# Optimization experiments

Hardware: AMD Instinct MI355X
Metric: run time of the kernel (lower is better)

Reference implementation:

```python
import jax, jax.numpy as jnp
import numpy as np

BITS = 8
CLIP_BOUND = 2.0 ** (BITS - 1) - 1.0  # 127 for int8
EPS = 1e-12


def _per_tensor_scale(x):
    # Dynamic per-tensor abs-max calibration (TensorQuantizer.update with
    # calibration over the whole tensor): scale maps abs-max to the clip bound.
    amax = jnp.max(jnp.abs(x))
    return CLIP_BOUND / jnp.maximum(amax, EPS)


def setup_inputs() -> dict:
    key = jax.random.key(0)
    k1, k2 = jax.random.split(key)
    lhs = jax.random.normal(k1, (4096, 4096), dtype=jnp.float32)
    rhs = jax.random.normal(k2, (4096, 4096), dtype=jnp.float32)
    return {"lhs": lhs, "rhs": rhs}


def reference(lhs, rhs):
    # --- calibration (scales are statistics, no gradient flows through them) ---
    ls = _per_tensor_scale(lhs)
    rs = _per_tensor_scale(rhs)

    # --- quantize to int8 grid ---
    ql = jnp.clip(jnp.round(lhs * ls), -CLIP_BOUND, CLIP_BOUND).astype(jnp.int8)
    qr = jnp.clip(jnp.round(rhs * rs), -CLIP_BOUND, CLIP_BOUND).astype(jnp.int8)

    # --- integer dot_general with int32 accumulation (aqt_dot_general core) ---
    dimension_numbers = (((1,), (0,)), ((), ()))
    acc = jax.lax.dot_general(
        ql, qr, dimension_numbers, preferred_element_type=jnp.int32
    )

    # --- dequantize by product of scales ---
    out = acc.astype(jnp.float32) / (ls * rs)
    return out
```

## Files before the change

kernel.cpp:

```cpp
#include <hip/hip_runtime.h>
#include <stdint.h>


#define NROW 4096
#define NELEM (4096 * 4096)

typedef __attribute__((ext_vector_type(4))) int int32x4;
typedef __attribute__((ext_vector_type(16))) int int32x16;
typedef const __attribute__((address_space(1))) int8_t* gptr1_t;
typedef __attribute__((address_space(3))) int8_t* lptr3_t;

__global__ void absmax_both_kernel(const float* __restrict__ lhs,
                                   const float* __restrict__ rhs,
                                   unsigned* __restrict__ amax) {
    __shared__ float red[4];
    const int t = blockIdx.x & 1;
    const float4* x4 = (const float4*)(t ? rhs : lhs);
    const int bid = blockIdx.x >> 1;
    const int stride = (gridDim.x >> 1) * blockDim.x;
    int i = bid * blockDim.x + threadIdx.x;
    float m0 = 0.0f, m1 = 0.0f, m2 = 0.0f, m3 = 0.0f;
    for (; i + 3 * stride < NELEM / 4; i += 4 * stride) {
        float4 a = x4[i];
        float4 b = x4[i + stride];
        float4 c = x4[i + 2 * stride];
        float4 d = x4[i + 3 * stride];
        m0 = fmaxf(m0, fmaxf(fmaxf(fabsf(a.x), fabsf(a.y)),
                             fmaxf(fabsf(a.z), fabsf(a.w))));
        m1 = fmaxf(m1, fmaxf(fmaxf(fabsf(b.x), fabsf(b.y)),
                             fmaxf(fabsf(b.z), fabsf(b.w))));
        m2 = fmaxf(m2, fmaxf(fmaxf(fabsf(c.x), fabsf(c.y)),
                             fmaxf(fabsf(c.z), fabsf(c.w))));
        m3 = fmaxf(m3, fmaxf(fmaxf(fabsf(d.x), fabsf(d.y)),
                             fmaxf(fabsf(d.z), fabsf(d.w))));
    }
    for (; i < NELEM / 4; i += stride) {
        float4 a = x4[i];
        m0 = fmaxf(m0, fmaxf(fmaxf(fabsf(a.x), fabsf(a.y)),
                             fmaxf(fabsf(a.z), fabsf(a.w))));
    }
    float m = fmaxf(fmaxf(m0, m1), fmaxf(m2, m3));
    for (int off = 32; off > 0; off >>= 1)
        m = fmaxf(m, __shfl_down(m, off, 64));
    const int lane = threadIdx.x & 63, wave = threadIdx.x >> 6;
    if (lane == 0) red[wave] = m;
    __syncthreads();
    if (threadIdx.x == 0) {
        float b = fmaxf(fmaxf(red[0], red[1]), fmaxf(red[2], red[3]));
        atomicMax(amax + t, __float_as_uint(b));
    }
}

__device__ __forceinline__ int q8(float v, float s) {
    int r = __float2int_rn(v * s);
    r = r < -127 ? -127 : r;
    r = r > 127 ? 127 : r;
    return r;
}

__device__ __forceinline__ int pack4(float a, float b, float c, float d,
                                     float s) {
    return (q8(a, s) & 0xff) | ((q8(b, s) & 0xff) << 8) |
           ((q8(c, s) & 0xff) << 16) | ((q8(d, s) & 0xff) << 24);
}

__global__ void quant_kernel(const float* __restrict__ lhs,
                             const float* __restrict__ rhs,
                             int8_t* __restrict__ qA, int8_t* __restrict__ qT,
                             const unsigned* __restrict__ amax) {
    __shared__ int8_t sm[64][68];
    if (blockIdx.x < 4096) {
        const float s = 127.0f / fmaxf(__uint_as_float(amax[0]), 1e-12f);
        const int c = blockIdx.x * 256 + threadIdx.x;
        const int l = c & 63;
        const int ks_g = (c >> 6) & 127;
        const int mt_g = c >> 13;
        const int row = mt_g * 32 + (l & 31);
        const int kb = ks_g * 32 + (l >> 5) * 16;
        const float4* src = (const float4*)(lhs + (size_t)row * NROW + kb);
        float4 v0 = src[0], v1 = src[1], v2 = src[2], v3 = src[3];
        int4 w;
        w.x = pack4(v0.x, v0.y, v0.z, v0.w, s);
        w.y = pack4(v1.x, v1.y, v1.z, v1.w, s);
        w.z = pack4(v2.x, v2.y, v2.z, v2.w, s);
        w.w = pack4(v3.x, v3.y, v3.z, v3.w, s);
        *(int4*)(qA + (size_t)c * 16) = w;
    } else {
        const float s = 127.0f / fmaxf(__uint_as_float(amax[1]), 1e-12f);
        const int b = blockIdx.x - 4096;
        const int n0 = (b & 63) * 64, k0 = (b >> 6) * 64;
        const int rl = threadIdx.x >> 4;
        const int nq = threadIdx.x & 15;
        for (int r = 0; r < 4; ++r) {
            const int kl = r * 16 + rl;
            float4 v = *(const float4*)(rhs + (size_t)(k0 + kl) * NROW + n0 + nq * 4);
            sm[nq * 4 + 0][kl] = (int8_t)q8(v.x, s);
            sm[nq * 4 + 1][kl] = (int8_t)q8(v.y, s);
            sm[nq * 4 + 2][kl] = (int8_t)q8(v.z, s);
            sm[nq * 4 + 3][kl] = (int8_t)q8(v.w, s);
        }
        __syncthreads();
        const int nt_l = threadIdx.x >> 7;
        const int ks_l = (threadIdx.x >> 6) & 1;
        const int l = threadIdx.x & 63;
        const int n_loc = nt_l * 32 + (l & 31);
        const int k_loc = ks_l * 32 + (l >> 5) * 16;
        int4 w;
        w.x = *(const int*)&sm[n_loc][k_loc + 0];
        w.y = *(const int*)&sm[n_loc][k_loc + 4];
        w.z = *(const int*)&sm[n_loc][k_loc + 8];
        w.w = *(const int*)&sm[n_loc][k_loc + 12];
        const int nt_g = (b & 63) * 2 + nt_l;
        const int ks_g = (b >> 6) * 2 + ks_l;
        *(int4*)(qT + (((size_t)nt_g * 128 + ks_g) * 64 + l) * 16) = w;
    }
}

__global__ __launch_bounds__(256, 2) void gemm_i8_kernel(
    const int8_t* __restrict__ qA, const int8_t* __restrict__ qBT,
    float* __restrict__ out, const unsigned* __restrict__ amax) {
    __shared__ __align__(16) int8_t sA[2][32768];

    const int tid = threadIdx.x;
    const int lane = tid & 63;
    const int wn = tid >> 6;

    const int bid = blockIdx.y * 16 + blockIdx.x;
    const int swz = (bid & 7) * 64 + (bid >> 3);
    const int m0 = (swz >> 4) * 128, n0 = (swz & 15) * 256;

    const int rl = lane & 31;
    const int hi = lane >> 5;

    const gptr1_t pA0 = (gptr1_t)(qA + (size_t)(m0 / 32) * 131072 + tid * 16);
    int8_t* sAf = &sA[0][0];
    const int dst0 = tid * 16;

    auto stage = [&](int slot, int w1) {
#pragma unroll
        for (int h = 0; h < 2; ++h) {
            const int kb = (2 * w1 + h) * 4096;
#pragma unroll
            for (int j = 0; j < 4; ++j) {
                __builtin_amdgcn_global_load_lds(
                    pA0 + (size_t)j * 131072 + kb,
                    (lptr3_t)(sAf + slot * 32768 + h * 16384 + dst0 + j * 4096),
                    16, 0, 0);
            }
        }
    };

    const int8_t* pbW = qBT + (size_t)(n0 / 32 + wn * 2) * 131072 + lane * 16;

    int32x16 acc[4][2];
#pragma unroll
    for (int mt = 0; mt < 4; ++mt)
#pragma unroll
        for (int nt = 0; nt < 2; ++nt) acc[mt][nt] = (int32x16)(0);

    const int aBase = lane * 16;

    int32x4 B0[4], B1[4];

#define LOADB(B, KT, KS0)                                                     \
    {                                                                         \
        const int8_t* bp = pbW + (size_t)(KT)*4096 + (KS0)*1024;              \
        B[0] = *(const int32x4*)(bp);                                         \
        B[1] = *(const int32x4*)(bp + 1024);                                  \
        B[2] = *(const int32x4*)(bp + 131072);                                \
        B[3] = *(const int32x4*)(bp + 131072 + 1024);                         \
    }

#define HALF(APTR, B, KS0)                                                    \
    {                                                                         \
        _Pragma("unroll") for (int k = 0; k < 2; ++k) {                       \
            int32x4 af[4];                                                    \
            _Pragma("unroll") for (int mt = 0; mt < 4; ++mt) af[mt] =         \
                *(const int32x4*)((APTR) + aBase + mt * 4096 +                \
                                  ((KS0) + k) * 1024);                        \
            __builtin_amdgcn_s_setprio(1);                                    \
            _Pragma("unroll") for (int mt = 0; mt < 4; ++mt)                  \
                _Pragma("unroll") for (int nt = 0; nt < 2; ++nt)              \
                    acc[mt][nt] = __builtin_amdgcn_mfma_i32_32x32x32_i8(      \
                        af[mt], B[nt * 2 + k], acc[mt][nt], 0, 0, 0);         \
            __builtin_amdgcn_s_setprio(0);                                    \
        }                                                                     \
    }

    stage(0, 0);
    __builtin_amdgcn_sched_barrier(0);
    LOADB(B0, 0, 0)
    asm volatile("s_waitcnt vmcnt(0)" ::: "memory");
    __builtin_amdgcn_sched_barrier(0);
    __builtin_amdgcn_s_barrier();
    __builtin_amdgcn_sched_barrier(0);

#pragma unroll 1
    for (int w = 0; w < 15; ++w) {
        const int8_t* a0 = sAf + (w & 1) * 32768;
        const int8_t* a1 = a0 + 16384;
        stage((w + 1) & 1, w + 1);
        __builtin_amdgcn_sched_barrier(0);
        LOADB(B1, 2 * w, 2)
        HALF(a0, B0, 0)
        LOADB(B0, 2 * w + 1, 0)
        HALF(a0, B1, 2)
        LOADB(B1, 2 * w + 1, 2)
        HALF(a1, B0, 0)
        LOADB(B0, 2 * w + 2, 0)
        HALF(a1, B1, 2)
        asm volatile("s_waitcnt vmcnt(4)" ::: "memory");
        __builtin_amdgcn_sched_barrier(0);
        __builtin_amdgcn_s_barrier();
        __builtin_amdgcn_sched_barrier(0);
    }
    {
        const int8_t* a0 = sAf + 32768;
        const int8_t* a1 = a0 + 16384;
        LOADB(B1, 30, 2)
        HALF(a0, B0, 0)
        LOADB(B0, 31, 0)
        HALF(a0, B1, 2)
        LOADB(B1, 31, 2)
        HALF(a1, B0, 0)
        HALF(a1, B1, 2)
    }

    const float ls = 127.0f / fmaxf(__uint_as_float(amax[0]), 1e-12f);
    const float rs = 127.0f / fmaxf(__uint_as_float(amax[1]), 1e-12f);
    const float inv = 1.0f / (ls * rs);
#pragma unroll
    for (int mt = 0; mt < 4; ++mt)
#pragma unroll
        for (int nt = 0; nt < 2; ++nt)
#pragma unroll
            for (int reg = 0; reg < 16; ++reg) {
                const int row = m0 + mt * 32 + (reg & 3) + 8 * (reg >> 2) +
                                4 * hi;
                const int col = n0 + wn * 64 + nt * 32 + rl;
                out[(size_t)row * NROW + col] = (float)acc[mt][nt][reg] * inv;
            }
#undef LOADB
#undef HALF
}

extern "C" void kernel_launch(void* const* d_in, const int* in_sizes, int n_in,
                              void* d_out, int out_size, void* d_ws,
                              size_t ws_size, hipStream_t stream) {
    const float* lhs = (const float*)d_in[0];
    const float* rhs = (const float*)d_in[1];
    float* out = (float*)d_out;

    int8_t* qA = (int8_t*)d_ws;
    int8_t* qBT = qA + (size_t)16 * 1024 * 1024;
    unsigned* amax = (unsigned*)(qBT + (size_t)16 * 1024 * 1024);

    hipMemsetAsync(amax, 0, 8, stream);
    absmax_both_kernel<<<2048, 256, 0, stream>>>(lhs, rhs, amax);
    quant_kernel<<<4096 + 4096, 256, 0, stream>>>(lhs, rhs, qA, qBT, amax);
    gemm_i8_kernel<<<dim3(16, 32), 256, 0, stream>>>(qA, qBT, out, amax);
}
```

Baseline: 137.7 us.

## Fuse absmax and quantize kernels into one cooperative kernel with grid sync

```diff
diff --git a/kernel.cpp b/kernel.cpp
--- a/kernel.cpp
+++ b/kernel.cpp
@@ -1,5 +1,8 @@
 #include <hip/hip_runtime.h>
+#include <hip/hip_cooperative_groups.h>
 #include <stdint.h>
+
+namespace cg = cooperative_groups;
 
 
 #define NROW 4096
@@ -9,47 +12,6 @@
 typedef __attribute__((ext_vector_type(16))) int int32x16;
 typedef const __attribute__((address_space(1))) int8_t* gptr1_t;
 typedef __attribute__((address_space(3))) int8_t* lptr3_t;
-
-__global__ void absmax_both_kernel(const float* __restrict__ lhs,
-                                   const float* __restrict__ rhs,
-                                   unsigned* __restrict__ amax) {
-    __shared__ float red[4];
-    const int t = blockIdx.x & 1;
-    const float4* x4 = (const float4*)(t ? rhs : lhs);
-    const int bid = blockIdx.x >> 1;
-    const int stride = (gridDim.x >> 1) * blockDim.x;
-    int i = bid * blockDim.x + threadIdx.x;
-    float m0 = 0.0f, m1 = 0.0f, m2 = 0.0f, m3 = 0.0f;
-    for (; i + 3 * stride < NELEM / 4; i += 4 * stride) {
-        float4 a = x4[i];
-        float4 b = x4[i + stride];
-        float4 c = x4[i + 2 * stride];
-        float4 d = x4[i + 3 * stride];
-        m0 = fmaxf(m0, fmaxf(fmaxf(fabsf(a.x), fabsf(a.y)),
-                             fmaxf(fabsf(a.z), fabsf(a.w))));
-        m1 = fmaxf(m1, fmaxf(fmaxf(fabsf(b.x), fabsf(b.y)),
-                             fmaxf(fabsf(b.z), fabsf(b.w))));
-        m2 = fmaxf(m2, fmaxf(fmaxf(fabsf(c.x), fabsf(c.y)),
-                             fmaxf(fabsf(c.z), fabsf(c.w))));
-        m3 = fmaxf(m3, fmaxf(fmaxf(fabsf(d.x), fabsf(d.y)),
-                             fmaxf(fabsf(d.z), fabsf(d.w))));
-    }
-    for (; i < NELEM / 4; i += stride) {
-        float4 a = x4[i];
-        m0 = fmaxf(m0, fmaxf(fmaxf(fabsf(a.x), fabsf(a.y)),
-                             fmaxf(fabsf(a.z), fabsf(a.w))));
-    }
-    float m = fmaxf(fmaxf(m0, m1), fmaxf(m2, m3));
-    for (int off = 32; off > 0; off >>= 1)
-        m = fmaxf(m, __shfl_down(m, off, 64));
-    const int lane = threadIdx.x & 63, wave = threadIdx.x >> 6;
-    if (lane == 0) red[wave] = m;
-    __syncthreads();
-    if (threadIdx.x == 0) {
-        float b = fmaxf(fmaxf(red[0], red[1]), fmaxf(red[2], red[3]));
-        atomicMax(amax + t, __float_as_uint(b));
-    }
-}
 
 __device__ __forceinline__ int q8(float v, float s) {
     int r = __float2int_rn(v * s);
@@ -64,55 +26,106 @@
            ((q8(c, s) & 0xff) << 16) | ((q8(d, s) & 0xff) << 24);
 }
 
-__global__ void quant_kernel(const float* __restrict__ lhs,
-                             const float* __restrict__ rhs,
-                             int8_t* __restrict__ qA, int8_t* __restrict__ qT,
-                             const unsigned* __restrict__ amax) {
+__global__ void fused_pre_kernel(const float* __restrict__ lhs,
+                                 const float* __restrict__ rhs,
+                                 int8_t* __restrict__ qA,
+                                 int8_t* __restrict__ qT,
+                                 unsigned* __restrict__ amax) {
     __shared__ int8_t sm[64][68];
-    if (blockIdx.x < 4096) {
+    __shared__ float red[4];
+
+    {
+        const int t = blockIdx.x & 1;
+        const float4* x4 = (const float4*)(t ? rhs : lhs);
+        const int bid = blockIdx.x >> 1;
+        const int stride = (gridDim.x >> 1) * blockDim.x;
+        int i = bid * blockDim.x + threadIdx.x;
+        float m0 = 0.0f, m1 = 0.0f, m2 = 0.0f, m3 = 0.0f;
+        for (; i + 3 * stride < NELEM / 4; i += 4 * stride) {
+            float4 a = x4[i];
+            float4 b = x4[i + stride];
+            float4 c = x4[i + 2 * stride];
+            float4 d = x4[i + 3 * stride];
+            m0 = fmaxf(m0, fmaxf(fmaxf(fabsf(a.x), fabsf(a.y)),
+                                 fmaxf(fabsf(a.z), fabsf(a.w))));
+            m1 = fmaxf(m1, fmaxf(fmaxf(fabsf(b.x), fabsf(b.y)),
+                                 fmaxf(fabsf(b.z), fabsf(b.w))));
+            m2 = fmaxf(m2, fmaxf(fmaxf(fabsf(c.x), fabsf(c.y)),
+                                 fmaxf(fabsf(c.z), fabsf(c.w))));
+            m3 = fmaxf(m3, fmaxf(fmaxf(fabsf(d.x), fabsf(d.y)),
+                                 fmaxf(fabsf(d.z), fabsf(d.w))));
+        }
+        for (; i < NELEM / 4; i += stride) {
+            float4 a = x4[i];
+            m0 = fmaxf(m0, fmaxf(fmaxf(fabsf(a.x), fabsf(a.y)),
+                                 fmaxf(fabsf(a.z), fabsf(a.w))));
+        }
+        float m = fmaxf(fmaxf(m0, m1), fmaxf(m2, m3));
+        for (int off = 32; off > 0; off >>= 1)
+            m = fmaxf(m, __shfl_down(m, off, 64));
+        const int lane = threadIdx.x & 63, wave = threadIdx.x >> 6;
+        if (lane == 0) red[wave] = m;
+        __syncthreads();
+        if (threadIdx.x == 0) {
+            float b = fmaxf(fmaxf(red[0], red[1]), fmaxf(red[2], red[3]));
+            atomicMax(amax + t, __float_as_uint(b));
+        }
+    }
+
+    cg::this_grid().sync();
+
+    if (blockIdx.x < 512) {
         const float s = 127.0f / fmaxf(__uint_as_float(amax[0]), 1e-12f);
-        const int c = blockIdx.x * 256 + threadIdx.x;
-        const int l = c & 63;
-        const int ks_g = (c >> 6) & 127;
-        const int mt_g = c >> 13;
-        const int row = mt_g * 32 + (l & 31);
-        const int kb = ks_g * 32 + (l >> 5) * 16;
-        const float4* src = (const float4*)(lhs + (size_t)row * NROW + kb);
-        float4 v0 = src[0], v1 = src[1], v2 = src[2], v3 = src[3];
-        int4 w;
-        w.x = pack4(v0.x, v0.y, v0.z, v0.w, s);
-        w.y = pack4(v1.x, v1.y, v1.z, v1.w, s);
-        w.z = pack4(v2.x, v2.y, v2.z, v2.w, s);
-        w.w = pack4(v3.x, v3.y, v3.z, v3.w, s);
-        *(int4*)(qA + (size_t)c * 16) = w;
+#pragma unroll 1
+        for (int it = 0; it < 8; ++it) {
+            const int c = (blockIdx.x * 8 + it) * 256 + threadIdx.x;
+            const int l = c & 63;
+            const int ks_g = (c >> 6) & 127;
+            const int mt_g = c >> 13;
+            const int row = mt_g * 32 + (l & 31);
+            const int kb = ks_g * 32 + (l >> 5) * 16;
+            const float4* src = (const float4*)(lhs + (size_t)row * NROW + kb);
+            float4 v0 = src[0], v1 = src[1], v2 = src[2], v3 = src[3];
+            int4 w;
+            w.x = pack4(v0.x, v0.y, v0.z, v0.w, s);
+            w.y = pack4(v1.x, v1.y, v1.z, v1.w, s);
+            w.z = pack4(v2.x, v2.y, v2.z, v2.w, s);
+            w.w = pack4(v3.x, v3.y, v3.z, v3.w, s);
+            *(int4*)(qA + (size_t)c * 16) = w;
+        }
     } else {
         const float s = 127.0f / fmaxf(__uint_as_float(amax[1]), 1e-12f);
-        const int b = blockIdx.x - 4096;
-        const int n0 = (b & 63) * 64, k0 = (b >> 6) * 64;
-        const int rl = threadIdx.x >> 4;
-        const int nq = threadIdx.x & 15;
-        for (int r = 0; r < 4; ++r) {
-            const int kl = r * 16 + rl;
-            float4 v = *(const float4*)(rhs + (size_t)(k0 + kl) * NROW + n0 + nq * 4);
-            sm[nq * 4 + 0][kl] = (int8_t)q8(v.x, s);
-            sm[nq * 4 + 1][kl] = (int8_t)q8(v.y, s);
-            sm[nq * 4 + 2][kl] = (int8_t)q8(v.z, s);
-            sm[nq * 4 + 3][kl] = (int8_t)q8(v.w, s);
-        }
-        __syncthreads();
-        const int nt_l = threadIdx.x >> 7;
-        const int ks_l = (threadIdx.x >> 6) & 1;
-        const int l = threadIdx.x & 63;
-        const int n_loc = nt_l * 32 + (l & 31);
-        const int k_loc = ks_l * 32 + (l >> 5) * 16;
-        int4 w;
-        w.x = *(const int*)&sm[n_loc][k_loc + 0];
-        w.y = *(const int*)&sm[n_loc][k_loc + 4];
-        w.z = *(const int*)&sm[n_loc][k_loc + 8];
-        w.w = *(const int*)&sm[n_loc][k_loc + 12];
-        const int nt_g = (b & 63) * 2 + nt_l;
-        const int ks_g = (b >> 6) * 2 + ks_l;
-        *(int4*)(qT + (((size_t)nt_g * 128 + ks_g) * 64 + l) * 16) = w;
+#pragma unroll 1
+        for (int it = 0; it < 8; ++it) {
+            const int b = (blockIdx.x - 512) * 8 + it;
+            const int n0 = (b & 63) * 64, k0 = (b >> 6) * 64;
+            const int rl = threadIdx.x >> 4;
+            const int nq = threadIdx.x & 15;
+            for (int r = 0; r < 4; ++r) {
+                const int kl = r * 16 + rl;
+                float4 v = *(const float4*)(rhs + (size_t)(k0 + kl) * NROW +
+                                            n0 + nq * 4);
+                sm[nq * 4 + 0][kl] = (int8_t)q8(v.x, s);
+                sm[nq * 4 + 1][kl] = (int8_t)q8(v.y, s);
+                sm[nq * 4 + 2][kl] = (int8_t)q8(v.z, s);
+                sm[nq * 4 + 3][kl] = (int8_t)q8(v.w, s);
+            }
+            __syncthreads();
+            const int nt_l = threadIdx.x >> 7;
+            const int ks_l = (threadIdx.x >> 6) & 1;
+            const int l = threadIdx.x & 63;
+            const int n_loc = nt_l * 32 + (l & 31);
+            const int k_loc = ks_l * 32 + (l >> 5) * 16;
+            int4 w;
+            w.x = *(const int*)&sm[n_loc][k_loc + 0];
+            w.y = *(const int*)&sm[n_loc][k_loc + 4];
+            w.z = *(const int*)&sm[n_loc][k_loc + 8];
+            w.w = *(const int*)&sm[n_loc][k_loc + 12];
+            const int nt_g = (b & 63) * 2 + nt_l;
+            const int ks_g = (b >> 6) * 2 + ks_l;
+            *(int4*)(qT + (((size_t)nt_g * 128 + ks_g) * 64 + l) * 16) = w;
+            __syncthreads();
+        }
     }
 }
 
@@ -256,7 +269,11 @@
     unsigned* amax = (unsigned*)(qBT + (size_t)16 * 1024 * 1024);
 
     hipMemsetAsync(amax, 0, 8, stream);
-    absmax_both_kernel<<<2048, 256, 0, stream>>>(lhs, rhs, amax);
-    quant_kernel<<<4096 + 4096, 256, 0, stream>>>(lhs, rhs, qA, qBT, amax);
+
+    void* kargs[] = {(void*)&lhs, (void*)&rhs, (void*)&qA, (void*)&qBT,
+                     (void*)&amax};
+    hipLaunchCooperativeKernel((void*)fused_pre_kernel, dim3(1024), dim3(256),
+                               kargs, 0, stream);
+
     gemm_i8_kernel<<<dim3(16, 32), 256, 0, stream>>>(qA, qBT, out, amax);
 }
```

New measurement: 222.1 us. +61.2%, slower.
